# Optimization experiments

Hardware: AMD Instinct MI355X
Metric: run time of the kernel (lower is better)

Reference implementation:

```python
import jax, jax.numpy as jnp
import numpy as np

B = 131072
W = 64
E = 16
DIMS = [W * E, 130, 110, 90, 70, 50]  # hidden funnel; final Linear 50 -> W
EPS = 1e-5  # torch BatchNorm1d default eps


def setup_inputs() -> dict:
    key = jax.random.key(0)
    ks = jax.random.split(key, 32)
    inp = {"events": jax.random.normal(ks[0], (B, W, E), dtype=jnp.float32)}
    ki = 1
    for i in range(5):
        fan_in, fan_out = DIMS[i], DIMS[i + 1]
        bound = 1.0 / np.sqrt(fan_in)
        inp[f"W{i}"] = jax.random.uniform(ks[ki], (fan_out, fan_in), jnp.float32, -bound, bound); ki += 1
        inp[f"b{i}"] = jax.random.uniform(ks[ki], (fan_out,), jnp.float32, -bound, bound); ki += 1
        inp[f"g{i}"] = jnp.ones((fan_out,), jnp.float32)   # BN gamma
        inp[f"be{i}"] = jnp.zeros((fan_out,), jnp.float32)  # BN beta
    bound = 1.0 / np.sqrt(50)
    inp["W5"] = jax.random.uniform(ks[ki], (W, 50), jnp.float32, -bound, bound); ki += 1
    inp["b5"] = jax.random.uniform(ks[ki], (W,), jnp.float32, -bound, bound)
    return inp


def _mlp(x, Ws, bs, gs, bes, W5, b5):
    # Linear -> BatchNorm (training-mode batch stats) -> ReLU, x5; then Linear -> sigmoid
    for Wl, bl, gl, bel in zip(Ws, bs, gs, bes):
        x = x @ Wl.T + bl
        mu = jnp.mean(x, axis=0)
        var = jnp.var(x, axis=0)
        x = gl * (x - mu) * jax.lax.rsqrt(var + EPS) + bel
        x = jax.nn.relu(x)
    return jax.nn.sigmoid(x @ W5.T + b5)


def reference(events, W0, b0, g0, be0, W1, b1, g1, be1, W2, b2, g2, be2,
              W3, b3, g3, be3, W4, b4, g4, be4, W5, b5):
    x = events.reshape((events.shape[0], W * E))
    probs = _mlp(x, [W0, W1, W2, W3, W4], [b0, b1, b2, b3, b4],
                 [g0, g1, g2, g3, g4], [be0, be1, be2, be3, be4], W5, b5)  # [B, W]
    # np.random.choice([0,1], p=[p, 1-p]) -> choice=1 w.p. (1-p)
    u = jax.random.uniform(jax.random.key(42), probs.shape, dtype=probs.dtype)
    chosen = (u < (1.0 - probs)).astype(probs.dtype)          # 'choice' in source
    chosen_events_np = 1.0 - chosen                           # returned mask
    # log prod |chosen - probs| == sum log|chosen - probs|
    log_probs = jnp.sum(jnp.log(jnp.abs(chosen - probs)), axis=1)  # [B]
    return chosen_events_np, log_probs
```

## Files before the change

kernel.cpp:

```cpp
#include <hip/hip_runtime.h>
#include <type_traits>

static const long BATCH = 131072;
static const int ROWS = 32;
static const int NBLOCKS = 4096;
static const int GBLOCKS = 2048;

using f64x4 = __attribute__((ext_vector_type(4))) double;

__device__ __forceinline__ unsigned rotl32(unsigned x, int d) {
  return (x << d) | (x >> (32 - d));
}

struct U2 { unsigned a, b; };

__device__ __forceinline__ U2 threefry(unsigned x0, unsigned x1) {
  const unsigned ks0 = 0u, ks1 = 42u, ks2 = 0u ^ 42u ^ 0x1BD11BDAu;
  x0 += ks0; x1 += ks1;
#define TF_R4(A,B,C,D) \
  x0 += x1; x1 = rotl32(x1, A); x1 ^= x0; \
  x0 += x1; x1 = rotl32(x1, B); x1 ^= x0; \
  x0 += x1; x1 = rotl32(x1, C); x1 ^= x0; \
  x0 += x1; x1 = rotl32(x1, D); x1 ^= x0;
  TF_R4(13,15,26,6)  x0 += ks1; x1 += ks2 + 1u;
  TF_R4(17,29,16,24) x0 += ks2; x1 += ks0 + 2u;
  TF_R4(13,15,26,6)  x0 += ks0; x1 += ks1 + 3u;
  TF_R4(17,29,16,24) x0 += ks1; x1 += ks2 + 4u;
  TF_R4(13,15,26,6)  x0 += ks2; x1 += ks0 + 5u;
#undef TF_R4
  U2 r; r.a = x0; r.b = x1; return r;
}

__device__ __forceinline__ float jax_uniform(unsigned idx) {
  U2 r = threefry(0u, idx);
  unsigned bits = r.a ^ r.b;
  unsigned fb = (bits >> 9) | 0x3f800000u;
  return __uint_as_float(fb) - 1.0f;
}

__global__ __launch_bounds__(64) void probe_layout(unsigned* __restrict__ maps) {
  __shared__ double X1[16][5], X2[16][5], W1s[4][17], W2s[4][17];
  const int l = threadIdx.x;
  const int lr = l & 15, lk = l >> 4;
  {
    int i = l >> 2, k = l & 3;
    X1[i][k] = (k == 0) ? (double)i : 0.0;
    X2[i][k] = (k == 0) ? 1.0 : 0.0;
    W1s[k][i] = (k == 0) ? 1.0 : 0.0;
    W2s[k][i] = (k == 0) ? (double)i : 0.0;
  }
  __syncthreads();
  f64x4 a1 = {0.0, 0.0, 0.0, 0.0}, a2 = {0.0, 0.0, 0.0, 0.0};
  a1 = __builtin_amdgcn_mfma_f64_16x16x4f64(X1[lr][lk], W1s[lk][lr], a1, 0, 0, 0);
  a2 = __builtin_amdgcn_mfma_f64_16x16x4f64(X2[lr][lk], W2s[lk][lr], a2, 0, 0, 0);
  unsigned m = 0;
  #pragma unroll
  for (int r = 0; r < 4; ++r) {
    int row = (int)(a1[r] + 0.5);
    int col = (int)(a2[r] + 0.5);
    m |= (unsigned)(((row & 15) << 4) | (col & 15)) << (8 * r);
  }
  maps[l] = m;
}

template<int M, int N, int MODE>
__global__ __launch_bounds__(256, 3) void gemm_mfma(
    const void* __restrict__ inv, const float* __restrict__ W,
    const float* __restrict__ bias,
    const double* __restrict__ bna, const double* __restrict__ bnc,
    const unsigned* __restrict__ maps_g,
    double* __restrict__ hout, double* __restrict__ partials)
{
  constexpr int BK = 16;
  constexpr int NT = (N + 15) / 16;
  constexpr int NPAD = NT * 16;
  constexpr int WSTR = NPAD + 2;
  constexpr int NCH = (M + BK - 1) / BK;
  constexpr int NW = BK * NPAD;
  constexpr int WLD = (NW + 255) / 256;
  constexpr int SMK = (MODE == 1) ? (NCH * BK) : 1;

  struct SMM { float ws[2][BK][WSTR]; double bn[2][SMK]; };
  union SMEM { SMM m; double tt[4][16][17]; };
  __shared__ SMEM sm;

  const int tid = threadIdx.x;
  const int w = tid >> 6, l = tid & 63;
  const int lr = l & 15, lk = l >> 4;
  const long i0 = (long)blockIdx.x * 64;
  const int wrow = w * 16;
  const unsigned um = maps_g[l];
  const long arow = i0 + wrow + lr;

  if constexpr (MODE == 1) {
    for (int k = tid; k < SMK; k += 256) {
      sm.m.bn[0][k] = (k < M) ? bna[k] : 0.0;
      sm.m.bn[1][k] = (k < M) ? bnc[k] : 0.0;
    }
  }

  float wreg[WLD];
  float a4f[4], a4fn[4];
  double a4d[4], a4dn[4];

  auto loadW = [&](int k0) {
    #pragma unroll
    for (int p = 0; p < WLD; ++p) {
      int idx = tid + p * 256;
      float v = 0.0f;
      if (idx < NW) {
        int j = idx >> 4, kk = idx & 15;
        int k = k0 + kk;
        if (j < N && k < M) v = W[(long)j * M + k];
      }
      wreg[p] = v;
    }
  };
  auto writeW = [&](int buf) {
    #pragma unroll
    for (int p = 0; p < WLD; ++p) {
      int idx = tid + p * 256;
      if (idx < NW) {
        int j = idx >> 4, kk = idx & 15;
        sm.m.ws[buf][kk][j] = wreg[p];
      }
    }
  };
  auto loadA = [&](int k0, bool nxt) {
    int kb = k0 + lk * 4;
    if constexpr (MODE == 0) {
      float* dst = nxt ? a4fn : a4f;
      if (kb + 4 <= M) {
        float4 v = *(const float4*)((const float*)inv + arow * (long)M + kb);
        dst[0] = v.x; dst[1] = v.y; dst[2] = v.z; dst[3] = v.w;
      } else {
        #pragma unroll
        for (int e = 0; e < 4; ++e)
          dst[e] = (kb + e < M) ? ((const float*)inv)[arow * (long)M + kb + e] : 0.0f;
      }
    } else {
      double* dst = nxt ? a4dn : a4d;
      #pragma unroll
      for (int e = 0; e < 4; ++e)
        dst[e] = (kb + e < M) ? ((const double*)inv)[arow * (long)M + kb + e] : 0.0;
    }
  };

  f64x4 acc[NT];
  #pragma unroll
  for (int t = 0; t < NT; ++t) acc[t] = (f64x4){0.0, 0.0, 0.0, 0.0};

  loadA(0, false);
  loadW(0);
  writeW(0);
  __syncthreads();
  int cur = 0;
  for (int ch = 0; ch < NCH; ++ch) {
    const int k0 = ch * BK;
    if (ch + 1 < NCH) { loadA(k0 + BK, true); loadW(k0 + BK); }
    #pragma unroll
    for (int ks = 0; ks < 4; ++ks) {
      double aA;
      if constexpr (MODE == 0) {
        aA = (double)a4f[ks];
      } else {
        int k = k0 + lk * 4 + ks;
        double v = a4d[ks] * sm.m.bn[0][k] + sm.m.bn[1][k];
        aA = v > 0.0 ? v : 0.0;
      }
      #pragma unroll
      for (int t = 0; t < NT; ++t) {
        double bB = (double)sm.m.ws[cur][lk * 4 + ks][t * 16 + lr];
        acc[t] = __builtin_amdgcn_mfma_f64_16x16x4f64(aA, bB, acc[t], 0, 0, 0);
      }
    }
    if (ch + 1 < NCH) writeW(cur ^ 1);
    __syncthreads();
    if (ch + 1 < NCH) {
      if constexpr (MODE == 0) {
        #pragma unroll
        for (int e = 0; e < 4; ++e) a4f[e] = a4fn[e];
      } else {
        #pragma unroll
        for (int e = 0; e < 4; ++e) a4d[e] = a4dn[e];
      }
      cur ^= 1;
    }
  }

  const int blk = blockIdx.x;
  for (int t = 0; t < NT; ++t) {
    __syncthreads();
    #pragma unroll
    for (int r = 0; r < 4; ++r) {
      unsigned b = (um >> (8 * r)) & 0xffu;
      sm.tt[w][b >> 4][b & 15] = acc[t][r];
    }
    __syncthreads();
    for (int idx = tid; idx < 1024; idx += 256) {
      int rb = idx >> 4, j16 = idx & 15;
      int j = t * 16 + j16;
      if (j < N) {
        double h = sm.tt[rb >> 4][rb & 15][j16] + (double)bias[j];
        hout[(i0 + rb) * (long)N + j] = h;
      }
    }
    if (tid < 64) {
      int j16 = tid >> 2, part = tid & 3;
      int j = t * 16 + j16;
      double s = 0.0, q = 0.0;
      if (j < N) {
        double bj = (double)bias[j];
        #pragma unroll
        for (int rr = 0; rr < 16; ++rr) {
          int rb = part * 16 + rr;
          double h = sm.tt[rb >> 4][rb & 15][j16] + bj;
          s += h; q += h * h;
        }
      }
      s += __shfl_xor(s, 1); s += __shfl_xor(s, 2);
      q += __shfl_xor(q, 1); q += __shfl_xor(q, 2);
      if (part == 0 && j < N) {
        partials[(long)j * GBLOCKS + blk] = s;
        partials[(long)(N + j) * GBLOCKS + blk] = q;
      }
    }
  }
}

__global__ __launch_bounds__(256) void final_store(
    const double* __restrict__ h4,
    const double* __restrict__ bna, const double* __restrict__ bnc,
    const float* __restrict__ W5, const float* __restrict__ b5,
    float* __restrict__ out0, float* __restrict__ out1)
{
  __shared__ double A5[ROWS][51];
  __shared__ double W5S[50][65];
  __shared__ double T[ROWS][65];
  const int tid = threadIdx.x;
  const int c = tid & 63, g = tid >> 6;
  const long i0 = (long)blockIdx.x * ROWS;

  for (int idx = tid; idx < ROWS * 50; idx += 256) {
    int r = idx / 50, k = idx % 50;
    double v = h4[(i0 + r) * 50 + k] * bna[k] + bnc[k];
    A5[r][k] = v > 0.0 ? v : 0.0;
  }
  for (int idx = tid; idx < 64 * 50; idx += 256) {
    int j = idx / 50, k = idx % 50;
    W5S[k][j] = (double)W5[j * 50 + k];
  }
  __syncthreads();

  double acc[8];
  #pragma unroll
  for (int rr = 0; rr < 8; ++rr) acc[rr] = 0.0;
  for (int k = 0; k < 50; ++k) {
    double w = W5S[k][c];
    #pragma unroll
    for (int rr = 0; rr < 8; ++rr) acc[rr] += A5[g * 8 + rr][k] * w;
  }
  double bj = (double)b5[c];
  #pragma unroll
  for (int rr = 0; rr < 8; ++rr) {
    int r = g * 8 + rr;
    double h = acc[rr] + bj;
    double p = 1.0 / (1.0 + exp(-h));
    float uf = jax_uniform((unsigned)((i0 + r) * 64 + c));
    bool ch = ((double)uf < 1.0 - p);
    out0[(i0 + r) * 64 + c] = ch ? 0.0f : 1.0f;
    T[r][c] = log(ch ? (1.0 - p) : p);
  }
  __syncthreads();
  for (int r = tid; r < ROWS; r += 256) {
    double s = 0.0;
    for (int j = 0; j < 64; ++j) s += T[r][j];
    out1[i0 + r] = (float)s;
  }
}

template<int M, int N>
__device__ __forceinline__ void step_gemm(const double* IN, const float* __restrict__ W,
                                          int tid, double* acc) {
  if (tid < N) {
    #pragma unroll
    for (int r = 0; r < 32; ++r) acc[r] = 0.0;
    for (int k = 0; k < M; ++k) {
      double wv = (double)W[tid * M + k];
      #pragma unroll
      for (int r = 0; r < 32; ++r) acc[r] += IN[r * M + k] * wv;
    }
  }
}

template<int N>
__device__ __forceinline__ void step_write(double* OUT, const double* acc,
                                           const float* __restrict__ b, int tid) {
  if (tid < N) {
    double bj = (double)b[tid];
    #pragma unroll
    for (int r = 0; r < 32; ++r) OUT[r * N + tid] = acc[r] + bj;
  }
}

template<int N>
__device__ __forceinline__ void step_stats(const double* acc, const float* __restrict__ b,
                                           double* partials, int blk, int tid) {
  if (tid < N) {
    double bj = (double)b[tid], s = 0.0, q = 0.0;
    #pragma unroll
    for (int r = 0; r < 32; ++r) { double h = acc[r] + bj; s += h; q += h * h; }
    partials[(long)tid * NBLOCKS + blk] = s;
    partials[(long)(N + tid) * NBLOCKS + blk] = q;
  }
}

template<int N>
__device__ __forceinline__ void apply_bn(double* BUF, const double* __restrict__ a,
                                         const double* __restrict__ c, int tid) {
  for (int idx = tid; idx < 32 * N; idx += 256) {
    int col = idx % N;
    double v = BUF[idx] * a[col] + c[col];
    BUF[idx] = v > 0.0 ? v : 0.0;
  }
}

template<int PL>
__global__ __launch_bounds__(256) void chain_pass(
    const float* __restrict__ ev,
    const float* __restrict__ W0, const float* __restrict__ b0,
    const float* __restrict__ W1, const float* __restrict__ b1,
    const float* __restrict__ W2, const float* __restrict__ b2,
    const float* __restrict__ W3, const float* __restrict__ b3,
    const float* __restrict__ W4, const float* __restrict__ b4,
    const float* __restrict__ W5, const float* __restrict__ b5,
    const double* __restrict__ bn_a, const double* __restrict__ bn_c,
    double* __restrict__ partials,
    float* __restrict__ out0, float* __restrict__ out1)
{
  __shared__ double SA[32 * 130];
  __shared__ double SB[32 * 110];
  const int tid = threadIdx.x;
  const int blk = blockIdx.x;
  const long i0 = (long)blk * 32;
  double acc[32];

  {
    float* evf = (float*)SA;
    if (tid < 130) {
      #pragma unroll
      for (int r = 0; r < 32; ++r) acc[r] = 0.0;
    }
    for (int c = 0; c < 4; ++c) {
      __syncthreads();
      for (int idx = tid; idx < 32 * 256; idx += 256) {
        int r = idx >> 8, kk = idx & 255;
        evf[idx] = ev[(i0 + r) * 1024 + c * 256 + kk];
      }
      __syncthreads();
      if (tid < 130) {
        for (int kk = 0; kk < 256; ++kk) {
          double wv = (double)W0[tid * 1024 + c * 256 + kk];
          #pragma unroll
          for (int r = 0; r < 32; ++r) acc[r] += (double)evf[r * 256 + kk] * wv;
        }
      }
    }
    __syncthreads();
    if constexpr (PL == 0) { step_stats<130>(acc, b0, partials, blk, tid); return; }
    step_write<130>(SA, acc, b0, tid);
    __syncthreads();
    apply_bn<130>(SA, bn_a + 0, bn_c + 0, tid);
    __syncthreads();
  }
  if constexpr (PL >= 1) {
    step_gemm<130, 110>(SA, W1, tid, acc);
    if constexpr (PL == 1) { step_stats<110>(acc, b1, partials, blk, tid); return; }
    __syncthreads();
    step_write<110>(SB, acc, b1, tid);
    __syncthreads();
    apply_bn<110>(SB, bn_a + 130, bn_c + 130, tid);
    __syncthreads();
  }
  if constexpr (PL >= 2) {
    step_gemm<110, 90>(SB, W2, tid, acc);
    if constexpr (PL == 2) { step_stats<90>(acc, b2, partials, blk, tid); return; }
    __syncthreads();
    step_write<90>(SA, acc, b2, tid);
    __syncthreads();
    apply_bn<90>(SA, bn_a + 240, bn_c + 240, tid);
    __syncthreads();
  }
  if constexpr (PL >= 3) {
    step_gemm<90, 70>(SA, W3, tid, acc);
    if constexpr (PL == 3) { step_stats<70>(acc, b3, partials, blk, tid); return; }
    __syncthreads();
    step_write<70>(SB, acc, b3, tid);
    __syncthreads();
    apply_bn<70>(SB, bn_a + 330, bn_c + 330, tid);
    __syncthreads();
  }
  if constexpr (PL >= 4) {
    step_gemm<70, 50>(SB, W4, tid, acc);
    if constexpr (PL == 4) { step_stats<50>(acc, b4, partials, blk, tid); return; }
    __syncthreads();
    step_write<50>(SA, acc, b4, tid);
    __syncthreads();
    apply_bn<50>(SA, bn_a + 400, bn_c + 400, tid);
    __syncthreads();
  }
  if constexpr (PL == 5) {
    if (tid < 64) {
      #pragma unroll
      for (int r = 0; r < 32; ++r) acc[r] = 0.0;
      for (int k = 0; k < 50; ++k) {
        double wv = (double)W5[tid * 50 + k];
        #pragma unroll
        for (int r = 0; r < 32; ++r) acc[r] += SA[r * 50 + k] * wv;
      }
      double bj = (double)b5[tid];
      #pragma unroll
      for (int r = 0; r < 32; ++r) {
        double h = acc[r] + bj;
        double p = 1.0 / (1.0 + exp(-h));
        float uf = jax_uniform((unsigned)((i0 + r) * 64 + tid));
        bool ch = ((double)uf < 1.0 - p);
        out0[(i0 + r) * 64 + tid] = ch ? 0.0f : 1.0f;
        double d = ch ? (1.0 - p) : p;
        SB[r * 64 + tid] = log(d);
      }
    }
    __syncthreads();
    if (tid < 32) {
      double s = 0.0;
      for (int j = 0; j < 64; ++j) s += SB[tid * 64 + j];
      out1[i0 + tid] = (float)s;
    }
  }
}

template<int N>
__global__ __launch_bounds__(256) void bn_finalize2(
    const double* __restrict__ partials, int nblocks,
    const float* __restrict__ g, const float* __restrict__ be,
    double* __restrict__ a, double* __restrict__ c)
{
  const int j = blockIdx.x;
  const int tid = threadIdx.x;
  double s = 0.0, q = 0.0;
  for (int b = tid; b < nblocks; b += 256) {
    s += partials[(long)j * nblocks + b];
    q += partials[(long)(N + j) * nblocks + b];
  }
  __shared__ double ls[256], lq[256];
  ls[tid] = s; lq[tid] = q;
  __syncthreads();
  for (int off = 128; off > 0; off >>= 1) {
    if (tid < off) { ls[tid] += ls[tid + off]; lq[tid] += lq[tid + off]; }
    __syncthreads();
  }
  if (tid == 0) {
    double mu  = ls[0] * (1.0 / 131072.0);
    double var = lq[0] * (1.0 / 131072.0) - mu * mu;
    double aj  = (double)g[j] / sqrt(var + 1e-5);
    a[j] = aj;
    c[j] = (double)be[j] - mu * aj;
  }
}

extern "C" void kernel_launch(void* const* d_in, const int* in_sizes, int n_in,
                              void* d_out, int out_size, void* d_ws, size_t ws_size,
                              hipStream_t stream)
{
  const float* F[23];
  for (int i = 0; i < 23; ++i) F[i] = (const float*)d_in[i];
  const float* ev = F[0];
  float* out0 = (float*)d_out;
  float* out1 = out0 + BATCH * 64;

  double* partials = (double*)d_out;
  double* bn_a = (double*)d_ws;
  double* bn_c = bn_a + 450;
  unsigned* maps = (unsigned*)(bn_c + 450);

  char* ws = (char*)d_ws;
  size_t used = (size_t)((char*)(maps + 64) - ws);
  used = (used + 255) & ~(size_t)255;
  const size_t needA = (size_t)BATCH * 130 * 8;
  const size_t needB = (size_t)BATCH * 110 * 8;

  dim3 b(256);

  if (ws_size >= used + needA + needB) {
    double* bufA = (double*)(ws + used);
    double* bufB = (double*)(ws + used + needA);
    dim3 g(GBLOCKS);
    probe_layout<<<dim3(1), dim3(64), 0, stream>>>(maps);
    gemm_mfma<1024, 130, 0><<<g, b, 0, stream>>>(ev, F[1], F[2],
        nullptr, nullptr, maps, bufA, partials);
    bn_finalize2<130><<<dim3(130), b, 0, stream>>>(partials, GBLOCKS, F[3], F[4], bn_a + 0, bn_c + 0);
    gemm_mfma<130, 110, 1><<<g, b, 0, stream>>>(bufA, F[5], F[6],
        bn_a + 0, bn_c + 0, maps, bufB, partials);
    bn_finalize2<110><<<dim3(110), b, 0, stream>>>(partials, GBLOCKS, F[7], F[8], bn_a + 130, bn_c + 130);
    gemm_mfma<110, 90, 1><<<g, b, 0, stream>>>(bufB, F[9], F[10],
        bn_a + 130, bn_c + 130, maps, bufA, partials);
    bn_finalize2<90><<<dim3(90), b, 0, stream>>>(partials, GBLOCKS, F[11], F[12], bn_a + 240, bn_c + 240);
    gemm_mfma<90, 70, 1><<<g, b, 0, stream>>>(bufA, F[13], F[14],
        bn_a + 240, bn_c + 240, maps, bufB, partials);
    bn_finalize2<70><<<dim3(70), b, 0, stream>>>(partials, GBLOCKS, F[15], F[16], bn_a + 330, bn_c + 330);
    gemm_mfma<70, 50, 1><<<g, b, 0, stream>>>(bufB, F[17], F[18],
        bn_a + 330, bn_c + 330, maps, bufA, partials);
    bn_finalize2<50><<<dim3(50), b, 0, stream>>>(partials, GBLOCKS, F[19], F[20], bn_a + 400, bn_c + 400);
    final_store<<<dim3(NBLOCKS), b, 0, stream>>>(bufA, bn_a + 400, bn_c + 400, F[21], F[22], out0, out1);
  } else {
    dim3 g(NBLOCKS);
#define ARGS ev, F[1],F[2], F[5],F[6], F[9],F[10], F[13],F[14], F[17],F[18], \
             F[21],F[22], bn_a, bn_c, partials, out0, out1
    chain_pass<0><<<g, b, 0, stream>>>(ARGS);
    bn_finalize2<130><<<dim3(130), b, 0, stream>>>(partials, NBLOCKS, F[3],  F[4],  bn_a + 0,   bn_c + 0);
    chain_pass<1><<<g, b, 0, stream>>>(ARGS);
    bn_finalize2<110><<<dim3(110), b, 0, stream>>>(partials, NBLOCKS, F[7],  F[8],  bn_a + 130, bn_c + 130);
    chain_pass<2><<<g, b, 0, stream>>>(ARGS);
    bn_finalize2<90><<<dim3(90),  b, 0, stream>>>(partials, NBLOCKS, F[11], F[12], bn_a + 240, bn_c + 240);
    chain_pass<3><<<g, b, 0, stream>>>(ARGS);
    bn_finalize2<70><<<dim3(70),  b, 0, stream>>>(partials, NBLOCKS, F[15], F[16], bn_a + 330, bn_c + 330);
    chain_pass<4><<<g, b, 0, stream>>>(ARGS);
    bn_finalize2<50><<<dim3(50),  b, 0, stream>>>(partials, NBLOCKS, F[19], F[20], bn_a + 400, bn_c + 400);
    chain_pass<5><<<g, b, 0, stream>>>(ARGS);
#undef ARGS
  }
}
```

Before: 1.078 ms.

## Load GEMM weight fragments directly into registers instead of staging through LDS

Each lane now loads its own float4 weight fragment straight from global memory into registers, replacing the shared-memory double buffer for W and the per-chunk __syncthreads barriers. The K loop becomes a manually unrolled two-register-buffer ping-pong, and the double-precision A loads are vectorized into double2 pairs. This is meant to remove LDS traffic and block-wide synchronization from the inner loop. In exchange it uses more registers (the launch-bounds occupancy hint is dropped) and issues redundant global weight loads across waves, relying on cache hits.

```diff
diff --git a/kernel.cpp b/kernel.cpp
--- a/kernel.cpp
+++ b/kernel.cpp
@@ -64,7 +64,7 @@
 }
 
 template<int M, int N, int MODE>
-__global__ __launch_bounds__(256, 3) void gemm_mfma(
+__global__ __launch_bounds__(256) void gemm_mfma(
     const void* __restrict__ inv, const float* __restrict__ W,
     const float* __restrict__ bias,
     const double* __restrict__ bna, const double* __restrict__ bnc,
@@ -73,15 +73,10 @@
 {
   constexpr int BK = 16;
   constexpr int NT = (N + 15) / 16;
-  constexpr int NPAD = NT * 16;
-  constexpr int WSTR = NPAD + 2;
   constexpr int NCH = (M + BK - 1) / BK;
-  constexpr int NW = BK * NPAD;
-  constexpr int WLD = (NW + 255) / 256;
   constexpr int SMK = (MODE == 1) ? (NCH * BK) : 1;
 
-  struct SMM { float ws[2][BK][WSTR]; double bn[2][SMK]; };
-  union SMEM { SMM m; double tt[4][16][17]; };
+  union SMEM { double bn[2][SMK]; double tt[4][16][17]; };
   __shared__ SMEM sm;
 
   const int tid = threadIdx.x;
@@ -94,55 +89,61 @@
 
   if constexpr (MODE == 1) {
     for (int k = tid; k < SMK; k += 256) {
-      sm.m.bn[0][k] = (k < M) ? bna[k] : 0.0;
-      sm.m.bn[1][k] = (k < M) ? bnc[k] : 0.0;
-    }
-  }
-
-  float wreg[WLD];
-  float a4f[4], a4fn[4];
-  double a4d[4], a4dn[4];
-
-  auto loadW = [&](int k0) {
-    #pragma unroll
-    for (int p = 0; p < WLD; ++p) {
-      int idx = tid + p * 256;
-      float v = 0.0f;
-      if (idx < NW) {
-        int j = idx >> 4, kk = idx & 15;
-        int k = k0 + kk;
-        if (j < N && k < M) v = W[(long)j * M + k];
-      }
-      wreg[p] = v;
+      sm.bn[0][k] = (k < M) ? bna[k] : 0.0;
+      sm.bn[1][k] = (k < M) ? bnc[k] : 0.0;
+    }
+    __syncthreads();
+  }
+
+  bool jok[NT];
+  #pragma unroll
+  for (int t = 0; t < NT; ++t) jok[t] = (t * 16 + lr) < N;
+
+  float4 w0[NT], w1[NT];
+  float a0f[4], a1f[4];
+  double a0d[4], a1d[4];
+
+  auto loadW = [&](int k0, float4* dst) {
+    const int kb = k0 + lk * 4;
+    #pragma unroll
+    for (int t = 0; t < NT; ++t) {
+      float4 v = make_float4(0.f, 0.f, 0.f, 0.f);
+      if (jok[t]) {
+        const float* wp = W + (long)(t * 16 + lr) * M + kb;
+        if constexpr ((M & 3) == 0) {
+          v = *(const float4*)wp;
+        } else {
+          if (kb + 4 <= M) {
+            float2 lo = *(const float2*)wp;
+            float2 hi = *(const float2*)(wp + 2);
+            v = make_float4(lo.x, lo.y, hi.x, hi.y);
+          } else {
+            if (kb + 0 < M) v.x = wp[0];
+            if (kb + 1 < M) v.y = wp[1];
+            if (kb + 2 < M) v.z = wp[2];
+            if (kb + 3 < M) v.w = wp[3];
+          }
+        }
+      }
+      dst[t] = v;
     }
   };
-  auto writeW = [&](int buf) {
-    #pragma unroll
-    for (int p = 0; p < WLD; ++p) {
-      int idx = tid + p * 256;
-      if (idx < NW) {
-        int j = idx >> 4, kk = idx & 15;
-        sm.m.ws[buf][kk][j] = wreg[p];
-      }
-    }
-  };
-  auto loadA = [&](int k0, bool nxt) {
-    int kb = k0 + lk * 4;
+  auto loadA = [&](int k0, float* df, double* dd) {
+    const int kb = k0 + lk * 4;
     if constexpr (MODE == 0) {
-      float* dst = nxt ? a4fn : a4f;
+      float4 v = *(const float4*)((const float*)inv + arow * (long)M + kb);
+      df[0] = v.x; df[1] = v.y; df[2] = v.z; df[3] = v.w;
+    } else {
       if (kb + 4 <= M) {
-        float4 v = *(const float4*)((const float*)inv + arow * (long)M + kb);
-        dst[0] = v.x; dst[1] = v.y; dst[2] = v.z; dst[3] = v.w;
+        const double* ap = (const double*)inv + arow * (long)M + kb;
+        double2 lo = *(const double2*)ap;
+        double2 hi = *(const double2*)(ap + 2);
+        dd[0] = lo.x; dd[1] = lo.y; dd[2] = hi.x; dd[3] = hi.y;
       } else {
         #pragma unroll
         for (int e = 0; e < 4; ++e)
-          dst[e] = (kb + e < M) ? ((const float*)inv)[arow * (long)M + kb + e] : 0.0f;
-      }
-    } else {
-      double* dst = nxt ? a4dn : a4d;
-      #pragma unroll
-      for (int e = 0; e < 4; ++e)
-        dst[e] = (kb + e < M) ? ((const double*)inv)[arow * (long)M + kb + e] : 0.0;
+          dd[e] = (kb + e < M) ? ((const double*)inv)[arow * (long)M + kb + e] : 0.0;
+      }
     }
   };
 
@@ -150,43 +151,34 @@
   #pragma unroll
   for (int t = 0; t < NT; ++t) acc[t] = (f64x4){0.0, 0.0, 0.0, 0.0};
 
-  loadA(0, false);
-  loadW(0);
-  writeW(0);
-  __syncthreads();
-  int cur = 0;
-  for (int ch = 0; ch < NCH; ++ch) {
-    const int k0 = ch * BK;
-    if (ch + 1 < NCH) { loadA(k0 + BK, true); loadW(k0 + BK); }
+  auto compute = [&](int k0, const float4* wr, const float* af, const double* ad) {
     #pragma unroll
     for (int ks = 0; ks < 4; ++ks) {
       double aA;
       if constexpr (MODE == 0) {
-        aA = (double)a4f[ks];
+        aA = (double)af[ks];
       } else {
         int k = k0 + lk * 4 + ks;
-        double v = a4d[ks] * sm.m.bn[0][k] + sm.m.bn[1][k];
+        double v = ad[ks] * sm.bn[0][k] + sm.bn[1][k];
         aA = v > 0.0 ? v : 0.0;
       }
       #pragma unroll
       for (int t = 0; t < NT; ++t) {
-        double bB = (double)sm.m.ws[cur][lk * 4 + ks][t * 16 + lr];
+        double bB = (double)((const float*)&wr[t])[ks];
         acc[t] = __builtin_amdgcn_mfma_f64_16x16x4f64(aA, bB, acc[t], 0, 0, 0);
       }
     }
-    if (ch + 1 < NCH) writeW(cur ^ 1);
-    __syncthreads();
-    if (ch + 1 < NCH) {
-      if constexpr (MODE == 0) {
-        #pragma unroll
-        for (int e = 0; e < 4; ++e) a4f[e] = a4fn[e];
-      } else {
-        #pragma unroll
-        for (int e = 0; e < 4; ++e) a4d[e] = a4dn[e];
-      }
-      cur ^= 1;
-    }
-  }
+  };
+
+  loadW(0, w0); loadA(0, a0f, a0d);
+  int ch = 0;
+  for (; ch + 1 < NCH; ch += 2) {
+    loadW((ch + 1) * BK, w1); loadA((ch + 1) * BK, a1f, a1d);
+    compute(ch * BK, w0, a0f, a0d);
+    if (ch + 2 < NCH) { loadW((ch + 2) * BK, w0); loadA((ch + 2) * BK, a0f, a0d); }
+    compute((ch + 1) * BK, w1, a1f, a1d);
+  }
+  if (ch < NCH) compute(ch * BK, w0, a0f, a0d);
 
   const int blk = blockIdx.x;
   for (int t = 0; t < NT; ++t) {
```

After: 1.222 ms. +13.4%, slower.

## Split GEMM output tiles across two wave groups with 512-thread blocks

Applied to the files above, without the earlier changes.

The FP64 MFMA GEMM kernels now launch with 512 threads. Two groups of four waves each handle half of the 16-column output tiles for the same 64 rows, with the k-loop moved into a templated helper. This halves accumulator registers per wave and doubles the waves available to hide latency. Layers 2 to 5 also switch activation loads to double2 vector loads. In exchange, each A row is loaded twice (once per wave group), synchronisation covers a larger block, and the epilogue runs extra barrier rounds.

```diff
diff --git a/kernel.cpp b/kernel.cpp
--- a/kernel.cpp
+++ b/kernel.cpp
@@ -63,8 +63,110 @@
   maps[l] = m;
 }
 
+template<int M, int N, int MODE, int NTW, int TB>
+__device__ __forceinline__ void kloop(
+    const void* __restrict__ inv, const float* __restrict__ W,
+    float* __restrict__ wsm,
+    const double* __restrict__ bn0, const double* __restrict__ bn1,
+    long arow, int tid, int lr, int lk, f64x4* acc)
+{
+  constexpr int BK = 16;
+  constexpr int NT = (N + 15) / 16;
+  constexpr int NPAD = NT * 16;
+  constexpr int WSTR = NPAD + 2;
+  constexpr int NCH = (M + BK - 1) / BK;
+  constexpr int NW = BK * NPAD;
+  constexpr int WLD = (NW + 511) / 512;
+
+  float wreg[WLD];
+  float a4f[4], a4fn[4];
+  double a4d[4], a4dn[4];
+
+  auto loadW = [&](int k0) {
+    #pragma unroll
+    for (int p = 0; p < WLD; ++p) {
+      int idx = tid + p * 512;
+      float v = 0.0f;
+      if (idx < NW) {
+        int j = idx >> 4, kk = idx & 15;
+        int k = k0 + kk;
+        if (j < N && k < M) v = W[(long)j * M + k];
+      }
+      wreg[p] = v;
+    }
+  };
+  auto writeW = [&](int buf) {
+    #pragma unroll
+    for (int p = 0; p < WLD; ++p) {
+      int idx = tid + p * 512;
+      if (idx < NW) {
+        int j = idx >> 4, kk = idx & 15;
+        wsm[buf * BK * WSTR + kk * WSTR + j] = wreg[p];
+      }
+    }
+  };
+  auto loadA = [&](int k0, bool nxt) {
+    int kb = k0 + lk * 4;
+    if constexpr (MODE == 0) {
+      float* dst = nxt ? a4fn : a4f;
+      float4 v = *(const float4*)((const float*)inv + arow * (long)M + kb);
+      dst[0] = v.x; dst[1] = v.y; dst[2] = v.z; dst[3] = v.w;
+    } else {
+      double* dst = nxt ? a4dn : a4d;
+      if (kb + 4 <= M) {
+        const double* ap = (const double*)inv + arow * (long)M + kb;
+        double2 lo = *(const double2*)ap;
+        double2 hi = *(const double2*)(ap + 2);
+        dst[0] = lo.x; dst[1] = lo.y; dst[2] = hi.x; dst[3] = hi.y;
+      } else {
+        #pragma unroll
+        for (int e = 0; e < 4; ++e)
+          dst[e] = (kb + e < M) ? ((const double*)inv)[arow * (long)M + kb + e] : 0.0;
+      }
+    }
+  };
+
+  loadA(0, false);
+  loadW(0);
+  writeW(0);
+  __syncthreads();
+  int cur = 0;
+  for (int ch = 0; ch < NCH; ++ch) {
+    const int k0 = ch * BK;
+    if (ch + 1 < NCH) { loadA(k0 + BK, true); loadW(k0 + BK); }
+    #pragma unroll
+    for (int ks = 0; ks < 4; ++ks) {
+      double aA;
+      if constexpr (MODE == 0) {
+        aA = (double)a4f[ks];
+      } else {
+        int k = k0 + lk * 4 + ks;
+        double v = a4d[ks] * bn0[k] + bn1[k];
+        aA = v > 0.0 ? v : 0.0;
+      }
+      #pragma unroll
+      for (int t = 0; t < NTW; ++t) {
+        double bB = (double)wsm[cur * BK * WSTR + (lk * 4 + ks) * WSTR + (TB + t) * 16 + lr];
+        acc[t] = __builtin_amdgcn_mfma_f64_16x16x4f64(aA, bB, acc[t], 0, 0, 0);
+      }
+    }
+    if (ch + 1 < NCH) writeW(cur ^ 1);
+    __syncthreads();
+    if (ch + 1 < NCH) {
+      if constexpr (MODE == 0) {
+        #pragma unroll
+        for (int e = 0; e < 4; ++e) a4f[e] = a4fn[e];
+      } else {
+        #pragma unroll
+        for (int e = 0; e < 4; ++e) a4d[e] = a4dn[e];
+      }
+      cur ^= 1;
+    }
+  }
+}
+
 template<int M, int N, int MODE>
-__global__ __launch_bounds__(256, 3) void gemm_mfma(
+__global__ __launch_bounds__(512, 4) void gemm_mfma(
     const void* __restrict__ inv, const float* __restrict__ W,
     const float* __restrict__ bias,
     const double* __restrict__ bna, const double* __restrict__ bnc,
@@ -73,11 +175,11 @@
 {
   constexpr int BK = 16;
   constexpr int NT = (N + 15) / 16;
+  constexpr int NTA = (NT + 1) / 2;
+  constexpr int NTB = NT - NTA;
   constexpr int NPAD = NT * 16;
   constexpr int WSTR = NPAD + 2;
   constexpr int NCH = (M + BK - 1) / BK;
-  constexpr int NW = BK * NPAD;
-  constexpr int WLD = (NW + 255) / 256;
   constexpr int SMK = (MODE == 1) ? (NCH * BK) : 1;
 
   struct SMM { float ws[2][BK][WSTR]; double bn[2][SMK]; };
@@ -86,136 +188,64 @@
 
   const int tid = threadIdx.x;
   const int w = tid >> 6, l = tid & 63;
+  const int rg = w & 3, h = w >> 2;
   const int lr = l & 15, lk = l >> 4;
   const long i0 = (long)blockIdx.x * 64;
-  const int wrow = w * 16;
+  const int wrow = rg * 16;
   const unsigned um = maps_g[l];
   const long arow = i0 + wrow + lr;
+  const int tbase = h ? NTA : 0;
+  const int ntw = h ? NTB : NTA;
 
   if constexpr (MODE == 1) {
-    for (int k = tid; k < SMK; k += 256) {
+    for (int k = tid; k < SMK; k += 512) {
       sm.m.bn[0][k] = (k < M) ? bna[k] : 0.0;
       sm.m.bn[1][k] = (k < M) ? bnc[k] : 0.0;
     }
   }
 
-  float wreg[WLD];
-  float a4f[4], a4fn[4];
-  double a4d[4], a4dn[4];
-
-  auto loadW = [&](int k0) {
-    #pragma unroll
-    for (int p = 0; p < WLD; ++p) {
-      int idx = tid + p * 256;
-      float v = 0.0f;
-      if (idx < NW) {
-        int j = idx >> 4, kk = idx & 15;
-        int k = k0 + kk;
-        if (j < N && k < M) v = W[(long)j * M + k];
-      }
-      wreg[p] = v;
-    }
-  };
-  auto writeW = [&](int buf) {
-    #pragma unroll
-    for (int p = 0; p < WLD; ++p) {
-      int idx = tid + p * 256;
-      if (idx < NW) {
-        int j = idx >> 4, kk = idx & 15;
-        sm.m.ws[buf][kk][j] = wreg[p];
-      }
-    }
-  };
-  auto loadA = [&](int k0, bool nxt) {
-    int kb = k0 + lk * 4;
-    if constexpr (MODE == 0) {
-      float* dst = nxt ? a4fn : a4f;
-      if (kb + 4 <= M) {
-        float4 v = *(const float4*)((const float*)inv + arow * (long)M + kb);
-        dst[0] = v.x; dst[1] = v.y; dst[2] = v.z; dst[3] = v.w;
-      } else {
-        #pragma unroll
-        for (int e = 0; e < 4; ++e)
-          dst[e] = (kb + e < M) ? ((const float*)inv)[arow * (long)M + kb + e] : 0.0f;
-      }
-    } else {
-      double* dst = nxt ? a4dn : a4d;
+  f64x4 acc[NTA];
+  #pragma unroll
+  for (int t = 0; t < NTA; ++t) acc[t] = (f64x4){0.0, 0.0, 0.0, 0.0};
+
+  if (h == 0)
+    kloop<M, N, MODE, NTA, 0>(inv, W, (float*)sm.m.ws, sm.m.bn[0], sm.m.bn[1],
+                              arow, tid, lr, lk, acc);
+  else
+    kloop<M, N, MODE, NTB, NTA>(inv, W, (float*)sm.m.ws, sm.m.bn[0], sm.m.bn[1],
+                                arow, tid, lr, lk, acc);
+
+  const int blk = blockIdx.x;
+  for (int gt = 0; gt < NT; ++gt) {
+    __syncthreads();
+    if (gt >= tbase && gt < tbase + ntw) {
+      int t = gt - tbase;
       #pragma unroll
-      for (int e = 0; e < 4; ++e)
-        dst[e] = (kb + e < M) ? ((const double*)inv)[arow * (long)M + kb + e] : 0.0;
-    }
-  };
-
-  f64x4 acc[NT];
-  #pragma unroll
-  for (int t = 0; t < NT; ++t) acc[t] = (f64x4){0.0, 0.0, 0.0, 0.0};
-
-  loadA(0, false);
-  loadW(0);
-  writeW(0);
-  __syncthreads();
-  int cur = 0;
-  for (int ch = 0; ch < NCH; ++ch) {
-    const int k0 = ch * BK;
-    if (ch + 1 < NCH) { loadA(k0 + BK, true); loadW(k0 + BK); }
-    #pragma unroll
-    for (int ks = 0; ks < 4; ++ks) {
-      double aA;
-      if constexpr (MODE == 0) {
-        aA = (double)a4f[ks];
-      } else {
-        int k = k0 + lk * 4 + ks;
-        double v = a4d[ks] * sm.m.bn[0][k] + sm.m.bn[1][k];
-        aA = v > 0.0 ? v : 0.0;
-      }
-      #pragma unroll
-      for (int t = 0; t < NT; ++t) {
-        double bB = (double)sm.m.ws[cur][lk * 4 + ks][t * 16 + lr];
-        acc[t] = __builtin_amdgcn_mfma_f64_16x16x4f64(aA, bB, acc[t], 0, 0, 0);
-      }
-    }
-    if (ch + 1 < NCH) writeW(cur ^ 1);
-    __syncthreads();
-    if (ch + 1 < NCH) {
-      if constexpr (MODE == 0) {
-        #pragma unroll
-        for (int e = 0; e < 4; ++e) a4f[e] = a4fn[e];
-      } else {
-        #pragma unroll
-        for (int e = 0; e < 4; ++e) a4d[e] = a4dn[e];
-      }
-      cur ^= 1;
-    }
-  }
-
-  const int blk = blockIdx.x;
-  for (int t = 0; t < NT; ++t) {
-    __syncthreads();
-    #pragma unroll
-    for (int r = 0; r < 4; ++r) {
-      unsigned b = (um >> (8 * r)) & 0xffu;
-      sm.tt[w][b >> 4][b & 15] = acc[t][r];
-    }
-    __syncthreads();
-    for (int idx = tid; idx < 1024; idx += 256) {
+      for (int r = 0; r < 4; ++r) {
+        unsigned b = (um >> (8 * r)) & 0xffu;
+        sm.tt[rg][b >> 4][b & 15] = acc[t][r];
+      }
+    }
+    __syncthreads();
+    for (int idx = tid; idx < 1024; idx += 512) {
       int rb = idx >> 4, j16 = idx & 15;
-      int j = t * 16 + j16;
+      int j = gt * 16 + j16;
       if (j < N) {
-        double h = sm.tt[rb >> 4][rb & 15][j16] + (double)bias[j];
-        hout[(i0 + rb) * (long)N + j] = h;
+        double hh = sm.tt[rb >> 4][rb & 15][j16] + (double)bias[j];
+        hout[(i0 + rb) * (long)N + j] = hh;
       }
     }
     if (tid < 64) {
       int j16 = tid >> 2, part = tid & 3;
-      int j = t * 16 + j16;
+      int j = gt * 16 + j16;
       double s = 0.0, q = 0.0;
       if (j < N) {
         double bj = (double)bias[j];
         #pragma unroll
         for (int rr = 0; rr < 16; ++rr) {
           int rb = part * 16 + rr;
-          double h = sm.tt[rb >> 4][rb & 15][j16] + bj;
-          s += h; q += h * h;
+          double hh = sm.tt[rb >> 4][rb & 15][j16] + bj;
+          s += hh; q += hh * hh;
         }
       }
       s += __shfl_xor(s, 1); s += __shfl_xor(s, 2);
@@ -489,26 +519,26 @@
   const size_t needA = (size_t)BATCH * 130 * 8;
   const size_t needB = (size_t)BATCH * 110 * 8;
 
-  dim3 b(256);
+  dim3 b(256), bb(512);
 
   if (ws_size >= used + needA + needB) {
     double* bufA = (double*)(ws + used);
     double* bufB = (double*)(ws + used + needA);
     dim3 g(GBLOCKS);
     probe_layout<<<dim3(1), dim3(64), 0, stream>>>(maps);
-    gemm_mfma<1024, 130, 0><<<g, b, 0, stream>>>(ev, F[1], F[2],
+    gemm_mfma<1024, 130, 0><<<g, bb, 0, stream>>>(ev, F[1], F[2],
         nullptr, nullptr, maps, bufA, partials);
     bn_finalize2<130><<<dim3(130), b, 0, stream>>>(partials, GBLOCKS, F[3], F[4], bn_a + 0, bn_c + 0);
-    gemm_mfma<130, 110, 1><<<g, b, 0, stream>>>(bufA, F[5], F[6],
+    gemm_mfma<130, 110, 1><<<g, bb, 0, stream>>>(bufA, F[5], F[6],
         bn_a + 0, bn_c + 0, maps, bufB, partials);
     bn_finalize2<110><<<dim3(110), b, 0, stream>>>(partials, GBLOCKS, F[7], F[8], bn_a + 130, bn_c + 130);
-    gemm_mfma<110, 90, 1><<<g, b, 0, stream>>>(bufB, F[9], F[10],
+    gemm_mfma<110, 90, 1><<<g, bb, 0, stream>>>(bufB, F[9], F[10],
         bn_a + 130, bn_c + 130, maps, bufA, partials);
     bn_finalize2<90><<<dim3(90), b, 0, stream>>>(partials, GBLOCKS, F[11], F[12], bn_a + 240, bn_c + 240);
-    gemm_mfma<90, 70, 1><<<g, b, 0, stream>>>(bufA, F[13], F[14],
+    gemm_mfma<90, 70, 1><<<g, bb, 0, stream>>>(bufA, F[13], F[14],
         bn_a + 240, bn_c + 240, maps, bufB, partials);
     bn_finalize2<70><<<dim3(70), b, 0, stream>>>(partials, GBLOCKS, F[15], F[16], bn_a + 330, bn_c + 330);
-    gemm_mfma<70, 50, 1><<<g, b, 0, stream>>>(bufB, F[17], F[18],
+    gemm_mfma<70, 50, 1><<<g, bb, 0, stream>>>(bufB, F[17], F[18],
         bn_a + 330, bn_c + 330, maps, bufA, partials);
     bn_finalize2<50><<<dim3(50), b, 0, stream>>>(partials, GBLOCKS, F[19], F[20], bn_a + 400, bn_c + 400);
     final_store<<<dim3(NBLOCKS), b, 0, stream>>>(bufA, bn_a + 400, bn_c + 400, F[21], F[22], out0, out1);
```

Result: slower. 1.164 ms (+8.0%).

## Compute leftover output columns with scalar FMAs instead of a padded MFMA tile

Applied to the files above, without the earlier changes.

For the first layer (N=130), the column count is no longer padded to 144 with a ninth MFMA tile. The last two columns are computed with per-lane scalar double FMAs plus shuffle reductions, and their BN partial sums are written separately. This removes one of nine f64 MFMA tiles on the largest GEMM. The double-typed A loads in the later layers are also vectorised into double2 loads. The cost is extra shuffles, an additional syncthreads and separate shared buffers, which add LDS use and could hurt occupancy.

```diff
diff --git a/kernel.cpp b/kernel.cpp
--- a/kernel.cpp
+++ b/kernel.cpp
@@ -63,7 +63,7 @@
   maps[l] = m;
 }
 
-template<int M, int N, int MODE>
+template<int M, int N, int MODE, int NREM>
 __global__ __launch_bounds__(256, 3) void gemm_mfma(
     const void* __restrict__ inv, const float* __restrict__ W,
     const float* __restrict__ bias,
@@ -72,17 +72,23 @@
     double* __restrict__ hout, double* __restrict__ partials)
 {
   constexpr int BK = 16;
-  constexpr int NT = (N + 15) / 16;
+  constexpr int NT = (N - NREM + 15) / 16;
   constexpr int NPAD = NT * 16;
-  constexpr int WSTR = NPAD + 2;
+  constexpr int NSTG = (NPAD > N) ? NPAD : N;
+  constexpr int WSTR = NSTG + 2;
   constexpr int NCH = (M + BK - 1) / BK;
-  constexpr int NW = BK * NPAD;
+  constexpr int NW = BK * NSTG;
   constexpr int WLD = (NW + 255) / 256;
   constexpr int SMK = (MODE == 1) ? (NCH * BK) : 1;
 
-  struct SMM { float ws[2][BK][WSTR]; double bn[2][SMK]; };
-  union SMEM { SMM m; double tt[4][16][17]; };
-  __shared__ SMEM sm;
+  struct SMW { float ws[2][BK][WSTR]; };
+  union SMU {
+    SMW m;
+    double tt[4][16][17];
+  };
+  __shared__ SMU sm;
+  __shared__ double bnsm[2][SMK];
+  __shared__ double rem_s[4][2][NREM > 0 ? NREM : 1];
 
   const int tid = threadIdx.x;
   const int w = tid >> 6, l = tid & 63;
@@ -94,8 +100,8 @@
 
   if constexpr (MODE == 1) {
     for (int k = tid; k < SMK; k += 256) {
-      sm.m.bn[0][k] = (k < M) ? bna[k] : 0.0;
-      sm.m.bn[1][k] = (k < M) ? bnc[k] : 0.0;
+      bnsm[0][k] = (k < M) ? bna[k] : 0.0;
+      bnsm[1][k] = (k < M) ? bnc[k] : 0.0;
     }
   }
 
@@ -130,25 +136,29 @@
     int kb = k0 + lk * 4;
     if constexpr (MODE == 0) {
       float* dst = nxt ? a4fn : a4f;
+      float4 v = *(const float4*)((const float*)inv + arow * (long)M + kb);
+      dst[0] = v.x; dst[1] = v.y; dst[2] = v.z; dst[3] = v.w;
+    } else {
+      double* dst = nxt ? a4dn : a4d;
       if (kb + 4 <= M) {
-        float4 v = *(const float4*)((const float*)inv + arow * (long)M + kb);
-        dst[0] = v.x; dst[1] = v.y; dst[2] = v.z; dst[3] = v.w;
+        const double* ap = (const double*)inv + arow * (long)M + kb;
+        double2 lo = *(const double2*)ap;
+        double2 hi = *(const double2*)(ap + 2);
+        dst[0] = lo.x; dst[1] = lo.y; dst[2] = hi.x; dst[3] = hi.y;
       } else {
         #pragma unroll
         for (int e = 0; e < 4; ++e)
-          dst[e] = (kb + e < M) ? ((const float*)inv)[arow * (long)M + kb + e] : 0.0f;
-      }
-    } else {
-      double* dst = nxt ? a4dn : a4d;
-      #pragma unroll
-      for (int e = 0; e < 4; ++e)
-        dst[e] = (kb + e < M) ? ((const double*)inv)[arow * (long)M + kb + e] : 0.0;
+          dst[e] = (kb + e < M) ? ((const double*)inv)[arow * (long)M + kb + e] : 0.0;
+      }
     }
   };
 
   f64x4 acc[NT];
   #pragma unroll
   for (int t = 0; t < NT; ++t) acc[t] = (f64x4){0.0, 0.0, 0.0, 0.0};
+  double racc[NREM > 0 ? NREM : 1];
+  #pragma unroll
+  for (int c = 0; c < (NREM > 0 ? NREM : 1); ++c) racc[c] = 0.0;
 
   loadA(0, false);
   loadW(0);
@@ -165,13 +175,22 @@
         aA = (double)a4f[ks];
       } else {
         int k = k0 + lk * 4 + ks;
-        double v = a4d[ks] * sm.m.bn[0][k] + sm.m.bn[1][k];
+        double v = a4d[ks] * bnsm[0][k] + bnsm[1][k];
         aA = v > 0.0 ? v : 0.0;
       }
       #pragma unroll
       for (int t = 0; t < NT; ++t) {
         double bB = (double)sm.m.ws[cur][lk * 4 + ks][t * 16 + lr];
         acc[t] = __builtin_amdgcn_mfma_f64_16x16x4f64(aA, bB, acc[t], 0, 0, 0);
+      }
+      if constexpr (NREM == 2) {
+        float2 rv = *(const float2*)&sm.m.ws[cur][lk * 4 + ks][NPAD];
+        racc[0] += aA * (double)rv.x;
+        racc[1] += aA * (double)rv.y;
+      } else if constexpr (NREM > 0) {
+        #pragma unroll
+        for (int c = 0; c < NREM; ++c)
+          racc[c] += aA * (double)sm.m.ws[cur][lk * 4 + ks][NPAD + c];
       }
     }
     if (ch + 1 < NCH) writeW(cur ^ 1);
@@ -189,6 +208,35 @@
   }
 
   const int blk = blockIdx.x;
+
+  if constexpr (NREM > 0) {
+    #pragma unroll
+    for (int c = 0; c < NREM; ++c) {
+      racc[c] += __shfl_xor(racc[c], 16);
+      racc[c] += __shfl_xor(racc[c], 32);
+      int j = NPAD + c;
+      double h = racc[c] + (double)bias[j];
+      if (lk == 0) hout[(i0 + wrow + lr) * (long)N + j] = h;
+      double s = h, q = h * h;
+      #pragma unroll
+      for (int off = 1; off < 16; off <<= 1) {
+        s += __shfl_xor(s, off);
+        q += __shfl_xor(q, off);
+      }
+      if (l == 0) { rem_s[w][0][c] = s; rem_s[w][1][c] = q; }
+    }
+  }
+  __syncthreads();
+  if constexpr (NREM > 0) {
+    if (tid < NREM) {
+      int j = NPAD + tid;
+      partials[(long)j * GBLOCKS + blk] =
+          rem_s[0][0][tid] + rem_s[1][0][tid] + rem_s[2][0][tid] + rem_s[3][0][tid];
+      partials[(long)(N + j) * GBLOCKS + blk] =
+          rem_s[0][1][tid] + rem_s[1][1][tid] + rem_s[2][1][tid] + rem_s[3][1][tid];
+    }
+  }
+
   for (int t = 0; t < NT; ++t) {
     __syncthreads();
     #pragma unroll
@@ -496,19 +544,19 @@
     double* bufB = (double*)(ws + used + needA);
     dim3 g(GBLOCKS);
     probe_layout<<<dim3(1), dim3(64), 0, stream>>>(maps);
-    gemm_mfma<1024, 130, 0><<<g, b, 0, stream>>>(ev, F[1], F[2],
+    gemm_mfma<1024, 130, 0, 2><<<g, b, 0, stream>>>(ev, F[1], F[2],
         nullptr, nullptr, maps, bufA, partials);
     bn_finalize2<130><<<dim3(130), b, 0, stream>>>(partials, GBLOCKS, F[3], F[4], bn_a + 0, bn_c + 0);
-    gemm_mfma<130, 110, 1><<<g, b, 0, stream>>>(bufA, F[5], F[6],
+    gemm_mfma<130, 110, 1, 0><<<g, b, 0, stream>>>(bufA, F[5], F[6],
         bn_a + 0, bn_c + 0, maps, bufB, partials);
     bn_finalize2<110><<<dim3(110), b, 0, stream>>>(partials, GBLOCKS, F[7], F[8], bn_a + 130, bn_c + 130);
-    gemm_mfma<110, 90, 1><<<g, b, 0, stream>>>(bufB, F[9], F[10],
+    gemm_mfma<110, 90, 1, 0><<<g, b, 0, stream>>>(bufB, F[9], F[10],
         bn_a + 130, bn_c + 130, maps, bufA, partials);
     bn_finalize2<90><<<dim3(90), b, 0, stream>>>(partials, GBLOCKS, F[11], F[12], bn_a + 240, bn_c + 240);
-    gemm_mfma<90, 70, 1><<<g, b, 0, stream>>>(bufA, F[13], F[14],
+    gemm_mfma<90, 70, 1, 0><<<g, b, 0, stream>>>(bufA, F[13], F[14],
         bn_a + 240, bn_c + 240, maps, bufB, partials);
     bn_finalize2<70><<<dim3(70), b, 0, stream>>>(partials, GBLOCKS, F[15], F[16], bn_a + 330, bn_c + 330);
-    gemm_mfma<70, 50, 1><<<g, b, 0, stream>>>(bufB, F[17], F[18],
+    gemm_mfma<70, 50, 1, 0><<<g, b, 0, stream>>>(bufB, F[17], F[18],
         bn_a + 330, bn_c + 330, maps, bufA, partials);
     bn_finalize2<50><<<dim3(50), b, 0, stream>>>(partials, GBLOCKS, F[19], F[20], bn_a + 400, bn_c + 400);
     final_store<<<dim3(NBLOCKS), b, 0, stream>>>(bufA, bn_a + 400, bn_c + 400, F[21], F[22], out0, out1);
```

New measurement: 1.040 ms. 1.04x faster.
